# Kernel optimization log

Hardware: AMD Instinct MI355X
Metric: run time of the kernel (lower is better)

## Reference

```python
import jax, jax.numpy as jnp
import numpy as np

N_NODES = 100000
HIDDEN = 64
N_EDGES = 1600000


def _sage_conv(x, edge_index, Wl, Wr, b):
    # PyG SAGEConv (mean aggr): out_i = W_l @ mean_{j->i} x_j + W_r @ x_i + b
    src, dst = edge_index[0], edge_index[1]
    msg = x[src]                                      # [E, H] gather
    agg = jax.ops.segment_sum(msg, dst, num_segments=N_NODES)  # [N, H]
    deg = jax.ops.segment_sum(jnp.ones((msg.shape[0],), x.dtype), dst,
                              num_segments=N_NODES)
    agg = agg / jnp.maximum(deg, 1.0)[:, None]
    return agg @ Wl.T + x @ Wr.T + b


def setup_inputs() -> dict:
    key = jax.random.key(0)
    ks = jax.random.split(key, 8)
    s = 1.0 / np.sqrt(HIDDEN)
    return {
        "emb": jax.random.normal(ks[0], (N_NODES, HIDDEN), jnp.float32),
        "Wl1": jax.random.normal(ks[1], (HIDDEN, HIDDEN), jnp.float32) * s,
        "Wr1": jax.random.normal(ks[2], (HIDDEN, HIDDEN), jnp.float32) * s,
        "b1": jnp.zeros((HIDDEN,), jnp.float32),
        "Wl2": jax.random.normal(ks[3], (HIDDEN, HIDDEN), jnp.float32) * s,
        "Wr2": jax.random.normal(ks[4], (HIDDEN, HIDDEN), jnp.float32) * s,
        "b2": jnp.zeros((HIDDEN,), jnp.float32),
        "node_id": jnp.arange(N_NODES, dtype=jnp.int64 if jax.config.jax_enable_x64 else jnp.int32),
        "edge_index": jax.random.randint(ks[5], (2, N_EDGES), 0, N_NODES),
    }


def reference(emb, Wl1, Wr1, b1, Wl2, Wr2, b2, node_id, edge_index):
    # Embedding lookup
    x = emb[node_id]                                   # [N, H]
    # GNN: relu(conv1) -> conv2
    x = jax.nn.relu(_sage_conv(x, edge_index, Wl1, Wr1, b1))
    x = _sage_conv(x, edge_index, Wl2, Wr2, b2)
    # Classifier: per-edge dot product of endpoint features
    ef1 = x[edge_index[0]]                             # [E, H]
    ef2 = x[edge_index[1]]                             # [E, H]
    return (ef1 * ef2).sum(axis=-1)                    # [E]
```

## Files before the change

kernel.cpp:

```cpp
#include <hip/hip_runtime.h>

#define N_NODES 100000
#define HID 64
#define N_EDGES 1600000
#define NB 391
#define C_EPB 6400
#define G_GATHER 6250

typedef __attribute__((ext_vector_type(8))) short bf16x8;
typedef __attribute__((ext_vector_type(4))) float f32x4;

__device__ __forceinline__ unsigned short f2bf(float f) {
    unsigned u = __float_as_uint(f);
    u = (u + 0x7FFFu + ((u >> 16) & 1u)) >> 16;
    return (unsigned short)u;
}
__device__ __forceinline__ float bflo(unsigned w) { return __uint_as_float(w << 16); }
__device__ __forceinline__ float bfhi(unsigned w) { return __uint_as_float(w & 0xFFFF0000u); }

__device__ __forceinline__ void acc8(float* a, uint4 u) {
    a[0] += bflo(u.x); a[1] += bfhi(u.x);
    a[2] += bflo(u.y); a[3] += bfhi(u.y);
    a[4] += bflo(u.z); a[5] += bfhi(u.z);
    a[6] += bflo(u.w); a[7] += bfhi(u.w);
}

__global__ void gather_hist_kernel(const float* __restrict__ emb,
                                   const int* __restrict__ nid,
                                   unsigned short* __restrict__ xh,
                                   const int* __restrict__ dst,
                                   int* __restrict__ bhist) {
    __shared__ int h[NB];
    if (blockIdx.x < G_GATHER) {
        int i = blockIdx.x * blockDim.x + threadIdx.x;
        int row = i >> 4;
        int c   = i & 15;
        int s   = nid[row];
        float4 v = reinterpret_cast<const float4*>(emb)[(size_t)s * 16 + c];
        uint2 p;
        p.x = (unsigned)f2bf(v.x) | ((unsigned)f2bf(v.y) << 16);
        p.y = (unsigned)f2bf(v.z) | ((unsigned)f2bf(v.w) << 16);
        reinterpret_cast<uint2*>(xh)[(size_t)row * 16 + c] = p;
    } else {
        int hb = blockIdx.x - G_GATHER;
        for (int i = threadIdx.x; i < NB; i += blockDim.x) h[i] = 0;
        __syncthreads();
        int nt = 256 * blockDim.x;
        const int4* d4 = (const int4*)dst;
        for (int q = hb * blockDim.x + threadIdx.x; q < N_EDGES / 4; q += nt) {
            int4 v = d4[q];
            atomicAdd(&h[v.x >> 8], 1);
            atomicAdd(&h[v.y >> 8], 1);
            atomicAdd(&h[v.z >> 8], 1);
            atomicAdd(&h[v.w >> 8], 1);
        }
        __syncthreads();
        for (int i = threadIdx.x; i < NB; i += blockDim.x)
            if (h[i]) atomicAdd(&bhist[i], h[i]);
    }
}

__global__ void bucket_scan(const int* __restrict__ bhist,
                            int* __restrict__ boff,
                            int* __restrict__ bcursor) {
    __shared__ int s[512];
    int v = (threadIdx.x < NB) ? bhist[threadIdx.x] : 0;
    s[threadIdx.x] = v;
    __syncthreads();
    for (int off = 1; off < 512; off <<= 1) {
        int t = (threadIdx.x >= off) ? s[threadIdx.x - off] : 0;
        __syncthreads();
        s[threadIdx.x] += t;
        __syncthreads();
    }
    if (threadIdx.x < NB) {
        int ex = s[threadIdx.x] - v;
        boff[threadIdx.x] = ex;
        bcursor[threadIdx.x] = ex;
    }
}

__global__ void bucket_scatter(const int* __restrict__ src,
                               const int* __restrict__ dst,
                               int* __restrict__ bcursor,
                               int2* __restrict__ pairs) {
    __shared__ int h[NB];
    __shared__ int base[NB];
    for (int i = threadIdx.x; i < NB; i += blockDim.x) h[i] = 0;
    __syncthreads();
    int q0 = blockIdx.x * (C_EPB / 4);
    int q1 = q0 + (C_EPB / 4);
    const int4* d4 = (const int4*)dst;
    const int4* s4 = (const int4*)src;
    for (int q = q0 + threadIdx.x; q < q1; q += blockDim.x) {
        int4 v = d4[q];
        atomicAdd(&h[v.x >> 8], 1);
        atomicAdd(&h[v.y >> 8], 1);
        atomicAdd(&h[v.z >> 8], 1);
        atomicAdd(&h[v.w >> 8], 1);
    }
    __syncthreads();
    for (int i = threadIdx.x; i < NB; i += blockDim.x) {
        int c = h[i];
        base[i] = c ? atomicAdd(&bcursor[i], c) : 0;
    }
    __syncthreads();
    for (int i = threadIdx.x; i < NB; i += blockDim.x) h[i] = 0;
    __syncthreads();
    for (int q = q0 + threadIdx.x; q < q1; q += blockDim.x) {
        int4 d = d4[q];
        int4 s = s4[q];
        int b, slot;
        b = d.x >> 8; slot = base[b] + atomicAdd(&h[b], 1); pairs[slot] = make_int2(s.x, d.x);
        b = d.y >> 8; slot = base[b] + atomicAdd(&h[b], 1); pairs[slot] = make_int2(s.y, d.y);
        b = d.z >> 8; slot = base[b] + atomicAdd(&h[b], 1); pairs[slot] = make_int2(s.z, d.z);
        b = d.w >> 8; slot = base[b] + atomicAdd(&h[b], 1); pairs[slot] = make_int2(s.w, d.w);
    }
}

__global__ void bucket_csr(const int2* __restrict__ pairs,
                           const int* __restrict__ boff,
                           const int* __restrict__ bcursor,
                           int* __restrict__ row_start,
                           int* __restrict__ adj) {
    __shared__ int cnt[256];
    __shared__ int sc[256];
    int b = blockIdx.x;
    int node0 = b << 8;
    int p0 = boff[b];
    int p1 = bcursor[b];
    int t = threadIdx.x;
    cnt[t] = 0;
    __syncthreads();
    for (int p = p0 + t; p < p1; p += 256)
        atomicAdd(&cnt[pairs[p].y & 255], 1);
    __syncthreads();
    int v = cnt[t];
    sc[t] = v;
    __syncthreads();
    for (int off = 1; off < 256; off <<= 1) {
        int u = (t >= off) ? sc[t - off] : 0;
        __syncthreads();
        sc[t] += u;
        __syncthreads();
    }
    sc[t] = p0 + sc[t] - v;
    __syncthreads();
    int node = node0 + t;
    if (node <= N_NODES) row_start[node] = sc[t];
    __syncthreads();
    for (int p = p0 + t; p < p1; p += 256) {
        int2 pr = pairs[p];
        int slot = atomicAdd(&sc[pr.y & 255], 1);
        adj[slot] = pr.x;
    }
}

__global__ void sage_fused(const int* __restrict__ row_start,
                           const int* __restrict__ adj,
                           const unsigned short* __restrict__ xh,
                           const float* __restrict__ Wl,
                           const float* __restrict__ Wr,
                           const float* __restrict__ bias,
                           unsigned short* __restrict__ H,
                           int relu) {
    int lane = threadIdx.x & 63;
    int m = lane & 15, quad = lane >> 4;

    bf16x8 wf[2][2][4];
    for (int mat = 0; mat < 2; ++mat) {
        const float* W = mat ? Wr : Wl;
        for (int ks = 0; ks < 2; ++ks)
            for (int ct = 0; ct < 4; ++ct) {
                const float* p = W + (ct * 16 + m) * HID + ks * 32 + quad * 8;
                bf16x8 f;
                #pragma unroll
                for (int j = 0; j < 8; ++j) f[j] = (short)f2bf(p[j]);
                wf[mat][ks][ct] = f;
            }
    }
    float bv[4];
    #pragma unroll
    for (int ct = 0; ct < 4; ++ct) bv[ct] = bias[ct * 16 + m];

    int wpb = blockDim.x >> 6;
    int wid = blockIdx.x * wpb + (threadIdx.x >> 6);
    int stride = gridDim.x * wpb;
    const int NT = N_NODES / 16;
    const uint4* x4 = (const uint4*)xh;

    for (int t = wid; t < NT; t += stride) {
        int row = t * 16 + m;
        int beg = row_start[row], end = row_start[row + 1];
        float ag[16];
        #pragma unroll
        for (int i = 0; i < 16; ++i) ag[i] = 0.f;

        int j = beg;
        for (; j + 3 < end; j += 4) {
            int s0 = adj[j], s1 = adj[j + 1], s2 = adj[j + 2], s3 = adj[j + 3];
            uint4 a0 = x4[(size_t)s0 * 8 + quad];
            uint4 b0 = x4[(size_t)s0 * 8 + 4 + quad];
            uint4 a1 = x4[(size_t)s1 * 8 + quad];
            uint4 b1 = x4[(size_t)s1 * 8 + 4 + quad];
            uint4 a2 = x4[(size_t)s2 * 8 + quad];
            uint4 b2 = x4[(size_t)s2 * 8 + 4 + quad];
            uint4 a3 = x4[(size_t)s3 * 8 + quad];
            uint4 b3 = x4[(size_t)s3 * 8 + 4 + quad];
            acc8(ag, a0); acc8(ag + 8, b0);
            acc8(ag, a1); acc8(ag + 8, b1);
            acc8(ag, a2); acc8(ag + 8, b2);
            acc8(ag, a3); acc8(ag + 8, b3);
        }
        for (; j < end; ++j) {
            int s = adj[j];
            acc8(ag,     x4[(size_t)s * 8 + quad]);
            acc8(ag + 8, x4[(size_t)s * 8 + 4 + quad]);
        }

        float inv = 1.0f / fmaxf((float)(end - beg), 1.0f);
        bf16x8 am0, am1, as0, as1;
        #pragma unroll
        for (int i = 0; i < 8; ++i) {
            am0[i] = (short)f2bf(ag[i] * inv);
            am1[i] = (short)f2bf(ag[8 + i] * inv);
        }
        as0 = *(const bf16x8*)(xh + (size_t)row * HID + quad * 8);
        as1 = *(const bf16x8*)(xh + (size_t)row * HID + 32 + quad * 8);

        f32x4 acc[4] = {{0,0,0,0},{0,0,0,0},{0,0,0,0},{0,0,0,0}};
        #pragma unroll
        for (int ct = 0; ct < 4; ++ct) {
            acc[ct] = __builtin_amdgcn_mfma_f32_16x16x32_bf16(am0, wf[0][0][ct], acc[ct], 0, 0, 0);
            acc[ct] = __builtin_amdgcn_mfma_f32_16x16x32_bf16(am1, wf[0][1][ct], acc[ct], 0, 0, 0);
            acc[ct] = __builtin_amdgcn_mfma_f32_16x16x32_bf16(as0, wf[1][0][ct], acc[ct], 0, 0, 0);
            acc[ct] = __builtin_amdgcn_mfma_f32_16x16x32_bf16(as1, wf[1][1][ct], acc[ct], 0, 0, 0);
        }
        #pragma unroll
        for (int ct = 0; ct < 4; ++ct) {
            #pragma unroll
            for (int r = 0; r < 4; ++r) {
                float v = acc[ct][r] + bv[ct];
                if (relu) v = fmaxf(v, 0.f);
                H[((size_t)t * 16 + quad * 4 + r) * HID + ct * 16 + m] = f2bf(v);
            }
        }
    }
}

__global__ void edge_dot_kernel(const int* __restrict__ src,
                                const int* __restrict__ dst,
                                const unsigned short* __restrict__ h,
                                float* __restrict__ out) {
    int t = blockIdx.x * blockDim.x + threadIdx.x;
    int g = t >> 3;
    int c = t & 7;
    int e0 = g * 2;
    if (e0 >= N_EDGES) return;
    int a0 = src[e0],     b0 = dst[e0];
    int a1 = src[e0 + 1], b1 = dst[e0 + 1];
    const uint4* h4 = reinterpret_cast<const uint4*>(h);
    uint4 va0 = h4[(size_t)a0 * 8 + c];
    uint4 vb0 = h4[(size_t)b0 * 8 + c];
    uint4 va1 = h4[(size_t)a1 * 8 + c];
    uint4 vb1 = h4[(size_t)b1 * 8 + c];
    float p0 = bflo(va0.x) * bflo(vb0.x) + bfhi(va0.x) * bfhi(vb0.x)
             + bflo(va0.y) * bflo(vb0.y) + bfhi(va0.y) * bfhi(vb0.y)
             + bflo(va0.z) * bflo(vb0.z) + bfhi(va0.z) * bfhi(vb0.z)
             + bflo(va0.w) * bflo(vb0.w) + bfhi(va0.w) * bfhi(vb0.w);
    float p1 = bflo(va1.x) * bflo(vb1.x) + bfhi(va1.x) * bfhi(vb1.x)
             + bflo(va1.y) * bflo(vb1.y) + bfhi(va1.y) * bfhi(vb1.y)
             + bflo(va1.z) * bflo(vb1.z) + bfhi(va1.z) * bfhi(vb1.z)
             + bflo(va1.w) * bflo(vb1.w) + bfhi(va1.w) * bfhi(vb1.w);
    p0 += __shfl_xor(p0, 1); p0 += __shfl_xor(p0, 2); p0 += __shfl_xor(p0, 4);
    p1 += __shfl_xor(p1, 1); p1 += __shfl_xor(p1, 2); p1 += __shfl_xor(p1, 4);
    if (c == 0) reinterpret_cast<float2*>(out)[g] = make_float2(p0, p1);
}

extern "C" void kernel_launch(void* const* d_in, const int* in_sizes, int n_in,
                              void* d_out, int out_size, void* d_ws, size_t ws_size,
                              hipStream_t stream) {
    const float* emb = (const float*)d_in[0];
    const float* Wl1 = (const float*)d_in[1];
    const float* Wr1 = (const float*)d_in[2];
    const float* b1  = (const float*)d_in[3];
    const float* Wl2 = (const float*)d_in[4];
    const float* Wr2 = (const float*)d_in[5];
    const float* b2  = (const float*)d_in[6];
    const int*   nid = (const int*)d_in[7];
    const int*   ei  = (const int*)d_in[8];
    const int* esrc = ei;
    const int* edst = ei + N_EDGES;
    float* out = (float*)d_out;

    const size_t NH = (size_t)N_NODES * HID;
    unsigned short* xh  = (unsigned short*)d_ws;
    unsigned short* h1h = xh + NH;
    unsigned short* h2h = h1h + NH;
    int* ib        = (int*)(h2h + NH);
    int* row_start = ib;
    int* adj       = ib + N_NODES + 64;
    int2* pairs    = (int2*)(adj + N_EDGES + 64);
    int* bhist     = (int*)(pairs + N_EDGES);
    int* boff      = bhist + NB + 1;
    int* bcursor   = boff + NB + 1;

    hipMemsetAsync(bhist, 0, NB * sizeof(int), stream);

    gather_hist_kernel<<<G_GATHER + 256, 256, 0, stream>>>(emb, nid, xh, edst, bhist);

    bucket_scan<<<1, 512, 0, stream>>>(bhist, boff, bcursor);
    bucket_scatter<<<N_EDGES / C_EPB, 256, 0, stream>>>(esrc, edst, bcursor, pairs);
    bucket_csr<<<NB, 256, 0, stream>>>(pairs, boff, bcursor, row_start, adj);

    sage_fused<<<1024, 256, 0, stream>>>(row_start, adj, xh,  Wl1, Wr1, b1, h1h, 1);
    sage_fused<<<1024, 256, 0, stream>>>(row_start, adj, h1h, Wl2, Wr2, b2, h2h, 0);

    edge_dot_kernel<<<((size_t)(N_EDGES / 2) * 8 + 255) / 256, 256, 0, stream>>>(esrc, edst, h2h, out);
}
```

Before: 312.8 us.

## Aggregate neighbors one row at a time per wave with LDS-staged MFMA operands

The SAGE kernel now has each wave process one 16-row tile row by row. Lanes are split into 4 neighbor slots × 16 feature chunks, so the neighbor gathers are coalesced 8-byte loads per row, and partial sums are combined with cross-lane shuffles. Aggregated rows are staged in LDS in MFMA fragment layout, and the bf16 weights are converted once per block into LDS instead of being held in registers. The grid becomes one tile per wave with no grid-stride loop. In exchange, each block pays an 8192-element weight conversion up front and adds a block barrier, and rows are walked serially within a wave.

```diff
diff --git a/kernel.cpp b/kernel.cpp
--- a/kernel.cpp
+++ b/kernel.cpp
@@ -6,6 +6,8 @@
 #define NB 391
 #define C_EPB 6400
 #define G_GATHER 6250
+#define NT 6250
+#define FUSE_BLOCKS ((NT + 3) / 4)
 
 typedef __attribute__((ext_vector_type(8))) short bf16x8;
 typedef __attribute__((ext_vector_type(4))) float f32x4;
@@ -17,13 +19,6 @@
 }
 __device__ __forceinline__ float bflo(unsigned w) { return __uint_as_float(w << 16); }
 __device__ __forceinline__ float bfhi(unsigned w) { return __uint_as_float(w & 0xFFFF0000u); }
-
-__device__ __forceinline__ void acc8(float* a, uint4 u) {
-    a[0] += bflo(u.x); a[1] += bfhi(u.x);
-    a[2] += bflo(u.y); a[3] += bfhi(u.y);
-    a[4] += bflo(u.z); a[5] += bfhi(u.z);
-    a[6] += bflo(u.w); a[7] += bfhi(u.w);
-}
 
 __global__ void gather_hist_kernel(const float* __restrict__ emb,
                                    const int* __restrict__ nid,
@@ -156,93 +151,104 @@
     }
 }
 
-__global__ void sage_fused(const int* __restrict__ row_start,
-                           const int* __restrict__ adj,
-                           const unsigned short* __restrict__ xh,
-                           const float* __restrict__ Wl,
-                           const float* __restrict__ Wr,
-                           const float* __restrict__ bias,
-                           unsigned short* __restrict__ H,
-                           int relu) {
+__global__ void __launch_bounds__(256, 6)
+sage_fused2(const int* __restrict__ row_start,
+            const int* __restrict__ adj,
+            const unsigned short* __restrict__ xh,
+            const float* __restrict__ Wl,
+            const float* __restrict__ Wr,
+            const float* __restrict__ bias,
+            unsigned short* __restrict__ H,
+            int relu) {
+    __shared__ uint4 sWq[1024];
+    __shared__ uint4 sAq[4 * 128];
+    unsigned short* sW = (unsigned short*)sWq;
+
+    for (int i = threadIdx.x; i < 8192; i += 256) {
+        int mat = i >> 12;
+        int nn  = (i >> 6) & 63;
+        int k   = i & 63;
+        const float* W = mat ? Wr : Wl;
+        sW[mat * 4096 + (k >> 3) * 512 + nn * 8 + (k & 7)] = f2bf(W[nn * 64 + k]);
+    }
+    __syncthreads();
+
     int lane = threadIdx.x & 63;
-    int m = lane & 15, quad = lane >> 4;
-
-    bf16x8 wf[2][2][4];
-    for (int mat = 0; mat < 2; ++mat) {
-        const float* W = mat ? Wr : Wl;
-        for (int ks = 0; ks < 2; ++ks)
-            for (int ct = 0; ct < 4; ++ct) {
-                const float* p = W + (ct * 16 + m) * HID + ks * 32 + quad * 8;
-                bf16x8 f;
-                #pragma unroll
-                for (int j = 0; j < 8; ++j) f[j] = (short)f2bf(p[j]);
-                wf[mat][ks][ct] = f;
+    int w    = threadIdx.x >> 6;
+    unsigned short* sA = (unsigned short*)(sAq + w * 128);
+
+    int tile = blockIdx.x * 4 + w;
+    int valid = tile < NT;
+
+    if (valid) {
+        int slot = lane >> 4;
+        int c    = lane & 15;
+        const uint2* xw = (const uint2*)xh;
+        for (int r = 0; r < 16; ++r) {
+            int row = tile * 16 + r;
+            int beg = row_start[row], end = row_start[row + 1];
+            float a0 = 0.f, a1 = 0.f, a2 = 0.f, a3 = 0.f;
+            int j = beg + slot;
+            for (; j + 12 < end; j += 16) {
+                int s0 = adj[j], s1 = adj[j + 4], s2 = adj[j + 8], s3 = adj[j + 12];
+                uint2 v0 = xw[(size_t)s0 * 16 + c];
+                uint2 v1 = xw[(size_t)s1 * 16 + c];
+                uint2 v2 = xw[(size_t)s2 * 16 + c];
+                uint2 v3 = xw[(size_t)s3 * 16 + c];
+                a0 += bflo(v0.x) + bflo(v1.x) + bflo(v2.x) + bflo(v3.x);
+                a1 += bfhi(v0.x) + bfhi(v1.x) + bfhi(v2.x) + bfhi(v3.x);
+                a2 += bflo(v0.y) + bflo(v1.y) + bflo(v2.y) + bflo(v3.y);
+                a3 += bfhi(v0.y) + bfhi(v1.y) + bfhi(v2.y) + bfhi(v3.y);
             }
-    }
-    float bv[4];
-    #pragma unroll
-    for (int ct = 0; ct < 4; ++ct) bv[ct] = bias[ct * 16 + m];
-
-    int wpb = blockDim.x >> 6;
-    int wid = blockIdx.x * wpb + (threadIdx.x >> 6);
-    int stride = gridDim.x * wpb;
-    const int NT = N_NODES / 16;
-    const uint4* x4 = (const uint4*)xh;
-
-    for (int t = wid; t < NT; t += stride) {
-        int row = t * 16 + m;
-        int beg = row_start[row], end = row_start[row + 1];
-        float ag[16];
-        #pragma unroll
-        for (int i = 0; i < 16; ++i) ag[i] = 0.f;
-
-        int j = beg;
-        for (; j + 3 < end; j += 4) {
-            int s0 = adj[j], s1 = adj[j + 1], s2 = adj[j + 2], s3 = adj[j + 3];
-            uint4 a0 = x4[(size_t)s0 * 8 + quad];
-            uint4 b0 = x4[(size_t)s0 * 8 + 4 + quad];
-            uint4 a1 = x4[(size_t)s1 * 8 + quad];
-            uint4 b1 = x4[(size_t)s1 * 8 + 4 + quad];
-            uint4 a2 = x4[(size_t)s2 * 8 + quad];
-            uint4 b2 = x4[(size_t)s2 * 8 + 4 + quad];
-            uint4 a3 = x4[(size_t)s3 * 8 + quad];
-            uint4 b3 = x4[(size_t)s3 * 8 + 4 + quad];
-            acc8(ag, a0); acc8(ag + 8, b0);
-            acc8(ag, a1); acc8(ag + 8, b1);
-            acc8(ag, a2); acc8(ag + 8, b2);
-            acc8(ag, a3); acc8(ag + 8, b3);
+            for (; j < end; j += 4) {
+                uint2 v = xw[(size_t)adj[j] * 16 + c];
+                a0 += bflo(v.x); a1 += bfhi(v.x);
+                a2 += bflo(v.y); a3 += bfhi(v.y);
+            }
+            a0 += __shfl_xor(a0, 16); a0 += __shfl_xor(a0, 32);
+            a1 += __shfl_xor(a1, 16); a1 += __shfl_xor(a1, 32);
+            a2 += __shfl_xor(a2, 16); a2 += __shfl_xor(a2, 32);
+            a3 += __shfl_xor(a3, 16); a3 += __shfl_xor(a3, 32);
+            if (slot == 0) {
+                float inv = 1.0f / fmaxf((float)(end - beg), 1.0f);
+                uint2 p;
+                p.x = (unsigned)f2bf(a0 * inv) | ((unsigned)f2bf(a1 * inv) << 16);
+                p.y = (unsigned)f2bf(a2 * inv) | ((unsigned)f2bf(a3 * inv) << 16);
+                *(uint2*)(sA + (c >> 1) * 128 + r * 8 + 4 * (c & 1)) = p;
+            }
         }
-        for (; j < end; ++j) {
-            int s = adj[j];
-            acc8(ag,     x4[(size_t)s * 8 + quad]);
-            acc8(ag + 8, x4[(size_t)s * 8 + 4 + quad]);
-        }
-
-        float inv = 1.0f / fmaxf((float)(end - beg), 1.0f);
-        bf16x8 am0, am1, as0, as1;
-        #pragma unroll
-        for (int i = 0; i < 8; ++i) {
-            am0[i] = (short)f2bf(ag[i] * inv);
-            am1[i] = (short)f2bf(ag[8 + i] * inv);
-        }
-        as0 = *(const bf16x8*)(xh + (size_t)row * HID + quad * 8);
-        as1 = *(const bf16x8*)(xh + (size_t)row * HID + 32 + quad * 8);
+    }
+    __syncthreads();
+
+    if (valid) {
+        int m = lane & 15, quad = lane >> 4;
+        bf16x8 am0 = *(const bf16x8*)(sA + (0 * 4 + quad) * 128 + m * 8);
+        bf16x8 am1 = *(const bf16x8*)(sA + (1 * 4 + quad) * 128 + m * 8);
+        size_t rowbase = ((size_t)tile * 16 + m) * HID;
+        bf16x8 as0 = *(const bf16x8*)(xh + rowbase + quad * 8);
+        bf16x8 as1 = *(const bf16x8*)(xh + rowbase + 32 + quad * 8);
 
         f32x4 acc[4] = {{0,0,0,0},{0,0,0,0},{0,0,0,0},{0,0,0,0}};
         #pragma unroll
         for (int ct = 0; ct < 4; ++ct) {
-            acc[ct] = __builtin_amdgcn_mfma_f32_16x16x32_bf16(am0, wf[0][0][ct], acc[ct], 0, 0, 0);
-            acc[ct] = __builtin_amdgcn_mfma_f32_16x16x32_bf16(am1, wf[0][1][ct], acc[ct], 0, 0, 0);
-            acc[ct] = __builtin_amdgcn_mfma_f32_16x16x32_bf16(as0, wf[1][0][ct], acc[ct], 0, 0, 0);
-            acc[ct] = __builtin_amdgcn_mfma_f32_16x16x32_bf16(as1, wf[1][1][ct], acc[ct], 0, 0, 0);
+            int n = ct * 16 + m;
+            bf16x8 bl0 = *(const bf16x8*)(sW + (0 * 4 + quad) * 512 + n * 8);
+            bf16x8 bl1 = *(const bf16x8*)(sW + (1 * 4 + quad) * 512 + n * 8);
+            bf16x8 br0 = *(const bf16x8*)(sW + 4096 + (0 * 4 + quad) * 512 + n * 8);
+            bf16x8 br1 = *(const bf16x8*)(sW + 4096 + (1 * 4 + quad) * 512 + n * 8);
+            acc[ct] = __builtin_amdgcn_mfma_f32_16x16x32_bf16(am0, bl0, acc[ct], 0, 0, 0);
+            acc[ct] = __builtin_amdgcn_mfma_f32_16x16x32_bf16(am1, bl1, acc[ct], 0, 0, 0);
+            acc[ct] = __builtin_amdgcn_mfma_f32_16x16x32_bf16(as0, br0, acc[ct], 0, 0, 0);
+            acc[ct] = __builtin_amdgcn_mfma_f32_16x16x32_bf16(as1, br1, acc[ct], 0, 0, 0);
         }
         #pragma unroll
         for (int ct = 0; ct < 4; ++ct) {
+            float bv = bias[ct * 16 + m];
             #pragma unroll
             for (int r = 0; r < 4; ++r) {
-                float v = acc[ct][r] + bv[ct];
+                float v = acc[ct][r] + bv;
                 if (relu) v = fmaxf(v, 0.f);
-                H[((size_t)t * 16 + quad * 4 + r) * HID + ct * 16 + m] = f2bf(v);
+                H[((size_t)tile * 16 + quad * 4 + r) * HID + ct * 16 + m] = f2bf(v);
             }
         }
     }
@@ -313,8 +319,8 @@
     bucket_scatter<<<N_EDGES / C_EPB, 256, 0, stream>>>(esrc, edst, bcursor, pairs);
     bucket_csr<<<NB, 256, 0, stream>>>(pairs, boff, bcursor, row_start, adj);
 
-    sage_fused<<<1024, 256, 0, stream>>>(row_start, adj, xh,  Wl1, Wr1, b1, h1h, 1);
-    sage_fused<<<1024, 256, 0, stream>>>(row_start, adj, h1h, Wl2, Wr2, b2, h2h, 0);
+    sage_fused2<<<FUSE_BLOCKS, 256, 0, stream>>>(row_start, adj, xh,  Wl1, Wr1, b1, h1h, 1);
+    sage_fused2<<<FUSE_BLOCKS, 256, 0, stream>>>(row_start, adj, h1h, Wl2, Wr2, b2, h2h, 0);
 
     edge_dot_kernel<<<((size_t)(N_EDGES / 2) * 8 + 255) / 256, 256, 0, stream>>>(esrc, edst, h2h, out);
 }
```

New measurement: 343.7 us. 9.9% more time.
